# Performance work log

Measured on AMD Instinct MI355X. Metric: run time of the kernel, lower is better.

Reference implementation:

```python
import jax, jax.numpy as jnp
import numpy as np
from jax import lax

# ---- static module constants (the torch module's registered buffers) ----
NRB = 8            # num_radial_basis
RAD = 2.5          # diameter / 2
GRID = 192         # voxel grid extent
N = 200000         # occupied voxels
DIM = 80           # 32x0e + 16x1o
ALPHA = 1.0 / np.sqrt(48.0)   # e3nn path normalization (fan_in = 32 + 16 into each output irrep)

_ax = np.arange(-2.0, 3.0, dtype=np.float32)                        # floor(2.5/1.0)=2 -> 5 taps/axis
LATTICE = np.stack(np.meshgrid(_ax, _ax, _ax, indexing='ij'), -1)   # [5,5,5,3]
PERM = np.arange(125).reshape(5, 5, 5).transpose(2, 1, 0).reshape(-1)  # einsum('xyz...->zyx...') as a flat permutation
OFFS = LATTICE.reshape(-1, 3).astype(np.int32)[PERM]                # voxel offsets, ordered to match permuted kernel


def _radial_emb():
    # soft_one_hot_linspace(..., basis='smooth_finite', cutoff=True)
    d = np.linalg.norm(LATTICE, axis=-1)
    centers = np.linspace(0.0, RAD, NRB + 2)[1:-1]
    step = centers[1] - centers[0]
    t = (d[..., None] - centers) / step
    inside = np.abs(t) < 1.0
    safe = np.where(inside, 1.0 - t * t, 1.0)
    return (1.14136 * np.exp(2.0) * np.where(inside, np.exp(-2.0 / safe), 0.0)).astype(np.float32)

EMB = _radial_emb().reshape(-1, NRB)  # [125, 8]


def _sph():
    # spherical harmonics l=0,1; normalize=True, normalization='component' (|Y_l|^2 = 2l+1)
    n = np.linalg.norm(LATTICE, axis=-1, keepdims=True)
    u = np.where(n > 0, LATTICE / np.maximum(n, 1e-9), 0.0)
    return np.concatenate([np.ones_like(n), np.sqrt(3.0) * u], -1).astype(np.float32)

SH = _sph().reshape(-1, 4)  # [125, 4]


def make_kernel(weight):
    # kernel(): (emb @ weight) / numel(lattice), then tp.right(sh, w) -> [tap, dim_in, dim_out]
    w = jnp.asarray(EMB) @ weight / 125.0        # [125, 2304]
    w1 = w[:, :1024].reshape(125, 32, 32)        # path 0e x 0e -> 0e
    w2 = w[:, 1024:1536].reshape(125, 32, 16)    # path 0e x 1o -> 1o
    w3 = w[:, 1536:1792].reshape(125, 16, 16)    # path 1o x 0e -> 1o
    w4 = w[:, 1792:].reshape(125, 16, 32)        # path 1o x 1o -> 0e (dot product)
    s0 = jnp.asarray(SH[:, 0])
    v = jnp.asarray(SH[:, 1:])
    eye3 = jnp.eye(3, dtype=w.dtype)
    K00 = ALPHA * w1 * s0[:, None, None]                                                  # [125,32,32]
    K01 = ALPHA * jnp.einsum('pik,pm->pikm', w2, v).reshape(125, 32, 48)                  # [125,32,48]
    K11 = ALPHA * jnp.einsum('pik,mn->pimkn', w3 * s0[:, None, None], eye3).reshape(125, 48, 48)
    K10 = (ALPHA / np.sqrt(3.0)) * jnp.einsum('pik,pm->pimk', w4, v).reshape(125, 48, 32)
    K = jnp.concatenate([jnp.concatenate([K00, K01], 2), jnp.concatenate([K10, K11], 2)], 1)
    return K[jnp.asarray(PERM)]  # xyz -> zyx tap order + flatten


def _forward(feats, weight, w_sc0, w_sc1, coords):
    kern = make_kernel(weight)  # [125, 80, 80]
    # residual e3nn Linear: per-irrep channel mixing with 1/sqrt(fan_in) normalization
    sc0 = feats[:, :32] @ (w_sc0 / np.sqrt(32.0))
    sc1 = jnp.einsum('nim,ik->nkm', feats[:, 32:].reshape(-1, 16, 3), w_sc1 / np.sqrt(16.0)).reshape(-1, 48)
    sc = jnp.concatenate([sc0, sc1], -1)
    # Minkowski sparse voxel conv: dense index volume -> per-tap gather / GEMM / accumulate
    n = coords.shape[0]
    idx_vol = jnp.full((GRID, GRID, GRID), -1, jnp.int32)
    idx_vol = idx_vol.at[coords[:, 0], coords[:, 1], coords[:, 2]].set(jnp.arange(n, dtype=jnp.int32))

    def tap(acc, oK):
        off, Ko = oK
        c = coords + off                                  # [N,3] neighbor coords for this tap
        ok = jnp.all((c >= 0) & (c < GRID), axis=1)
        cc = jnp.clip(c, 0, GRID - 1)
        nb = idx_vol[cc[:, 0], cc[:, 1], cc[:, 2]]        # [N] row index or -1
        f = jnp.where((ok & (nb >= 0))[:, None], feats[jnp.maximum(nb, 0)], 0.0)
        return acc + f @ Ko, None

    out, _ = lax.scan(tap, jnp.zeros(feats.shape, feats.dtype), (jnp.asarray(OFFS), kern))
    return sc + out


def setup_inputs() -> dict:
    key = jax.random.key(0)
    k1, k2, k3, k4 = jax.random.split(key, 4)
    rng = np.random.default_rng(0)
    lin = rng.choice(GRID ** 3, size=N, replace=False)  # unique occupied voxels
    coords = np.stack([lin // (GRID * GRID), (lin // GRID) % GRID, lin % GRID], 1).astype(np.int32)
    return {
        'feats': jax.random.normal(k1, (N, DIM), jnp.float32),
        'weight': jax.random.normal(k2, (NRB, 2304), jnp.float32),
        'w_sc0': jax.random.normal(k3, (32, 32), jnp.float32),
        'w_sc1': jax.random.normal(k4, (16, 16), jnp.float32),
        'coords': jnp.asarray(coords),
    }


def reference(feats, weight, w_sc0, w_sc1, coords):
    return _forward(feats, weight, w_sc0, w_sc1, coords)
```

## Files before the change

### kernel.cpp

```cpp
#include <hip/hip_runtime.h>

#define N_PTS 200000
#define GRIDL 192
#define CAP 8192
#define NREG 216
#define RCAP 1152
#define SCAP 96

#define VOL_OFF   0ull
#define VOL_BYTES (192ull*192ull*192ull*4ull)
#define BINS_OFF  28311552ull
#define BCNT_OFF  36503552ull
#define RCNT_OFF  36519552ull
#define PLIST_OFF 36547200ull
#define WBUF_OFF  38537856ull
#define VTAB_OFF  39689856ull
#define A0_OFF    39691856ull
#define A1_OFF    39695952ull

struct TapTable { int p[80]; };
__host__ __device__ constexpr TapTable make_taps() {
    TapTable tt{}; int t = 0;
    for (int a = -2; a <= 2; a++)
        for (int b = -2; b <= 2; b++)
            for (int c = -2; c <= 2; c++) {
                int sq = a*a + b*b + c*c;
                if (sq >= 1 && sq <= 6) tt.p[t++] = (a+2)*25 + (b+2)*5 + (c+2);
            }
    return tt;
}
__device__ const TapTable TAPS = make_taps();

__global__ void prep_kernel(const float* __restrict__ wt, const float* __restrict__ wsc0,
                            const float* __restrict__ wsc1, float* __restrict__ wbuf,
                            float* __restrict__ vtab, float* __restrict__ A0,
                            float* __restrict__ A1) {
    int p = blockIdx.x;
    int dx = p / 25 - 2, dy = (p / 5) % 5 - 2, dz = p % 5 - 2;
    double d = sqrt((double)(dx*dx + dy*dy + dz*dz));
    const double step = 2.5 / 9.0;
    const double cst = 1.14136 * exp(2.0);
    float emb[8];
#pragma unroll
    for (int r = 0; r < 8; r++) {
        double t = (d - (double)(r + 1) * step) / step;
        double tt = t * t;
        emb[r] = (tt < 1.0) ? (float)(cst * exp(-2.0 / (1.0 - tt))) : 0.0f;
    }
    if (threadIdx.x == 0) {
        float inv = (d > 0.0) ? (float)(sqrt(3.0) / d) : 0.0f;
        vtab[p*4+0] = dx * inv; vtab[p*4+1] = dy * inv;
        vtab[p*4+2] = dz * inv; vtab[p*4+3] = 0.0f;
    }
    const float ALPHA = 0.14433756729740643f;
    for (int q = threadIdx.x; q < 2304; q += blockDim.x) {
        float acc = 0.0f;
#pragma unroll
        for (int r = 0; r < 8; r++) acc = fmaf(emb[r], wt[r*2304 + q], acc);
        acc *= (1.0f / 125.0f);
        float val = acc * ((q < 1792) ? ALPHA : (1.0f / 12.0f));
        wbuf[p*2304 + q] = val;
        if (p == 62) {
            if (q < 1024)                   A0[q]        = wsc0[q] * 0.17677669529663687f + val;
            else if (q >= 1536 && q < 1792) A1[q-1536]   = wsc1[q-1536] * 0.25f + val;
        }
    }
}

__global__ __launch_bounds__(256) void scatter_kernel(const int* __restrict__ coords,
        int* __restrict__ vol, int* __restrict__ rcnt_pad, int2* __restrict__ plist) {
    __shared__ int hist[216];
    __shared__ int rbase[216];
    for (int i = threadIdx.x; i < 216; i += 256) hist[i] = 0;
    __syncthreads();
    for (int n = blockIdx.x * 256 + threadIdx.x; n < N_PTS; n += 65536) {
        int x = coords[n*3], y = coords[n*3+1], z = coords[n*3+2];
        vol[(x * GRIDL + y) * GRIDL + z] = n;
        int r = (x >> 5) * 36 + (y >> 5) * 6 + (z >> 5);
        atomicAdd(&hist[r], 1);
    }
    __syncthreads();
    if (threadIdx.x < 216) {
        rbase[threadIdx.x] = atomicAdd(&rcnt_pad[threadIdx.x * 32], hist[threadIdx.x]);
        hist[threadIdx.x] = 0;
    }
    __syncthreads();
    for (int n = blockIdx.x * 256 + threadIdx.x; n < N_PTS; n += 65536) {
        int x = coords[n*3], y = coords[n*3+1], z = coords[n*3+2];
        int r = (x >> 5) * 36 + (y >> 5) * 6 + (z >> 5);
        int j = rbase[r] + atomicAdd(&hist[r], 1);
        if (j < RCAP) plist[r * RCAP + j] = make_int2(n, (x << 16) | (y << 8) | z);
    }
}

__global__ __launch_bounds__(256) void enum_kernel(const int* __restrict__ vol,
        const int* __restrict__ rcnt_pad, const int2* __restrict__ plist,
        int* __restrict__ bcnt_pad, int2* __restrict__ bins) {
    int r = blockIdx.x;
    int cnt = min(rcnt_pad[r * 32], RCAP);
    __shared__ int hist[80];
    __shared__ int tbase[80];
    __shared__ int2 stage[80][SCAP];
    for (int i = threadIdx.x; i < 80; i += 256) hist[i] = 0;
    __syncthreads();
    for (int idx = threadIdx.x; idx < cnt; idx += 256) {
        int2 e = plist[r * RCAP + idx];
        int n = e.x, x = e.y >> 16, y = (e.y >> 8) & 255, z = e.y & 255;
        int t = 0;
#pragma unroll
        for (int a = -2; a <= 2; a++)
#pragma unroll
        for (int b = -2; b <= 2; b++)
#pragma unroll
        for (int c = -2; c <= 2; c++) {
            int sq = a*a + b*b + c*c;
            if (sq < 1 || sq > 6) continue;
            int cx = x + a, cy = y + b, cz = z + c;
            if (((unsigned)cx < 192u) && ((unsigned)cy < 192u) && ((unsigned)cz < 192u)) {
                int nb = vol[(cx * GRIDL + cy) * GRIDL + cz];
                if (nb >= 0) {
                    int j = atomicAdd(&hist[t], 1);
                    if (j < SCAP) stage[t][j] = make_int2(n, nb);
                }
            }
            t++;
        }
    }
    __syncthreads();
    if (threadIdx.x < 80) {
        int c = min(hist[threadIdx.x], SCAP);
        tbase[threadIdx.x] = atomicAdd(&bcnt_pad[TAPS.p[threadIdx.x] * 32], c);
    }
    __syncthreads();
    for (int t = 0; t < 80; t++) {
        int c = min(hist[t], SCAP);
        if (threadIdx.x < c) {
            int slot = tbase[t] + threadIdx.x;
            if (slot < CAP) bins[TAPS.p[t] * CAP + slot] = stage[t][threadIdx.x];
        }
    }
}

__global__ __launch_bounds__(256) void sc_self_kernel(const float* __restrict__ feats,
        const float* __restrict__ A0, const float* __restrict__ A1,
        float* __restrict__ out) {
    __shared__ __align__(16) float sA0[1024];
    __shared__ __align__(16) float sA1[256];
    for (int i = threadIdx.x; i < 1024; i += 256) sA0[i] = A0[i];
    if (threadIdx.x < 256) sA1[threadIdx.x] = A1[threadIdx.x];
    __syncthreads();
    int n = blockIdx.x * 256 + threadIdx.x;
    if (n >= N_PTS) return;
    const float4* fr = (const float4*)(feats + (size_t)n * 80);
    float4* orow = (float4*)(out + (size_t)n * 80);
    float f0[32];
#pragma unroll
    for (int j = 0; j < 8; j++) {
        float4 t = fr[j];
        f0[4*j] = t.x; f0[4*j+1] = t.y; f0[4*j+2] = t.z; f0[4*j+3] = t.w;
    }
    float a0[32];
#pragma unroll
    for (int k = 0; k < 32; k++) a0[k] = 0.0f;
#pragma unroll
    for (int i = 0; i < 32; i++) {
        float fv = f0[i];
#pragma unroll
        for (int k4 = 0; k4 < 8; k4++) {
            float4 w = ((const float4*)sA0)[i*8 + k4];
            a0[4*k4]   = fmaf(fv, w.x, a0[4*k4]);
            a0[4*k4+1] = fmaf(fv, w.y, a0[4*k4+1]);
            a0[4*k4+2] = fmaf(fv, w.z, a0[4*k4+2]);
            a0[4*k4+3] = fmaf(fv, w.w, a0[4*k4+3]);
        }
    }
#pragma unroll
    for (int j = 0; j < 8; j++) orow[j] = make_float4(a0[4*j], a0[4*j+1], a0[4*j+2], a0[4*j+3]);
    float f1[48];
#pragma unroll
    for (int j = 0; j < 12; j++) {
        float4 t = fr[8 + j];
        f1[4*j] = t.x; f1[4*j+1] = t.y; f1[4*j+2] = t.z; f1[4*j+3] = t.w;
    }
    float a1[48];
#pragma unroll
    for (int k = 0; k < 48; k++) a1[k] = 0.0f;
#pragma unroll
    for (int i = 0; i < 16; i++) {
        float fm0 = f1[3*i], fm1 = f1[3*i+1], fm2 = f1[3*i+2];
#pragma unroll
        for (int k4 = 0; k4 < 4; k4++) {
            float4 w = ((const float4*)sA1)[i*4 + k4];
            const float* wp = (const float*)&w;
#pragma unroll
            for (int kk = 0; kk < 4; kk++) {
                int k = 4*k4 + kk;
                a1[3*k]   = fmaf(fm0, wp[kk], a1[3*k]);
                a1[3*k+1] = fmaf(fm1, wp[kk], a1[3*k+1]);
                a1[3*k+2] = fmaf(fm2, wp[kk], a1[3*k+2]);
            }
        }
    }
#pragma unroll
    for (int j = 0; j < 12; j++) orow[8+j] = make_float4(a1[4*j], a1[4*j+1], a1[4*j+2], a1[4*j+3]);
}

__global__ __launch_bounds__(128) void bin_kernel(const float* __restrict__ feats,
        const float* __restrict__ wbuf, const float* __restrict__ vtab,
        const int* __restrict__ bcnt_pad, const int2* __restrict__ bins,
        float* __restrict__ out) {
    int p = blockIdx.x >> 4;
    int chunk = blockIdx.x & 15;
    int cnt = min(bcnt_pad[p * 32], CAP);
    int start = chunk * 512;
    if (start >= cnt) return;

    __shared__ __align__(16) float sW[2304];
    __shared__ float sv[4];
    __shared__ float ystage[2][64][81];
    __shared__ int   nst[2][64];

    for (int i = threadIdx.x; i < 2304; i += 128) sW[i] = wbuf[p*2304 + i];
    if (threadIdx.x < 4) sv[threadIdx.x] = vtab[p*4 + threadIdx.x];
    __syncthreads();

    int wv = threadIdx.x >> 6, lane = threadIdx.x & 63;
    const float4* sW1 = (const float4*)sW;
    const float4* sW2 = (const float4*)(sW + 1024);
    const float4* sW3 = (const float4*)(sW + 1536);
    const float4* sW4 = (const float4*)(sW + 1792);
    float v0 = sv[0], v1 = sv[1], v2 = sv[2];

    for (int it = 0; it < 4; it++) {
        int h = start + it * 128 + threadIdx.x;
        bool act = h < cnt;
        int n = -1, nb = 0;
        if (act) { int2 e = bins[p*CAP + h]; n = e.x; nb = e.y; }

        const float4* fr = (const float4*)(feats + (size_t)nb * 80);
        float f0[32], f1[48];
#pragma unroll
        for (int j = 0; j < 8; j++) {
            float4 t = fr[j];
            f0[4*j] = t.x; f0[4*j+1] = t.y; f0[4*j+2] = t.z; f0[4*j+3] = t.w;
        }
#pragma unroll
        for (int j = 0; j < 12; j++) {
            float4 t = fr[8 + j];
            f1[4*j] = t.x; f1[4*j+1] = t.y; f1[4*j+2] = t.z; f1[4*j+3] = t.w;
        }
        float g[16];
#pragma unroll
        for (int i = 0; i < 16; i++)
            g[i] = f1[3*i]*v0 + f1[3*i+1]*v1 + f1[3*i+2]*v2;

        float a0[32], cc[16];
#pragma unroll
        for (int k = 0; k < 32; k++) a0[k] = 0.0f;
#pragma unroll
        for (int k = 0; k < 16; k++) cc[k] = 0.0f;
#pragma unroll
        for (int i = 0; i < 32; i++) {
            float fv = f0[i];
#pragma unroll
            for (int k4 = 0; k4 < 8; k4++) {
                float4 w = sW1[i*8 + k4];
                a0[4*k4]   = fmaf(fv, w.x, a0[4*k4]);
                a0[4*k4+1] = fmaf(fv, w.y, a0[4*k4+1]);
                a0[4*k4+2] = fmaf(fv, w.z, a0[4*k4+2]);
                a0[4*k4+3] = fmaf(fv, w.w, a0[4*k4+3]);
            }
#pragma unroll
            for (int k4 = 0; k4 < 4; k4++) {
                float4 w = sW2[i*4 + k4];
                cc[4*k4]   = fmaf(fv, w.x, cc[4*k4]);
                cc[4*k4+1] = fmaf(fv, w.y, cc[4*k4+1]);
                cc[4*k4+2] = fmaf(fv, w.z, cc[4*k4+2]);
                cc[4*k4+3] = fmaf(fv, w.w, cc[4*k4+3]);
            }
        }
#pragma unroll
        for (int i = 0; i < 16; i++) {
            float gv = g[i];
#pragma unroll
            for (int k4 = 0; k4 < 8; k4++) {
                float4 w = sW4[i*8 + k4];
                a0[4*k4]   = fmaf(gv, w.x, a0[4*k4]);
                a0[4*k4+1] = fmaf(gv, w.y, a0[4*k4+1]);
                a0[4*k4+2] = fmaf(gv, w.z, a0[4*k4+2]);
                a0[4*k4+3] = fmaf(gv, w.w, a0[4*k4+3]);
            }
        }
#pragma unroll
        for (int k = 0; k < 32; k++) ystage[wv][lane][k] = a0[k];

        float a1[48];
#pragma unroll
        for (int k = 0; k < 16; k++) {
            a1[3*k] = v0 * cc[k]; a1[3*k+1] = v1 * cc[k]; a1[3*k+2] = v2 * cc[k];
        }
#pragma unroll
        for (int i = 0; i < 16; i++) {
            float fm0 = f1[3*i], fm1 = f1[3*i+1], fm2 = f1[3*i+2];
#pragma unroll
            for (int k4 = 0; k4 < 4; k4++) {
                float4 w = sW3[i*4 + k4];
                const float* wp = (const float*)&w;
#pragma unroll
                for (int kk = 0; kk < 4; kk++) {
                    int k = 4*k4 + kk;
                    a1[3*k]   = fmaf(fm0, wp[kk], a1[3*k]);
                    a1[3*k+1] = fmaf(fm1, wp[kk], a1[3*k+1]);
                    a1[3*k+2] = fmaf(fm2, wp[kk], a1[3*k+2]);
                }
            }
        }
#pragma unroll
        for (int k = 0; k < 48; k++) ystage[wv][lane][32 + k] = a1[k];
        nst[wv][lane] = act ? n : -1;
        __syncthreads();

        for (int h2 = 0; h2 < 64; h2++) {
            int nn = nst[wv][h2];
            if (nn < 0) continue;
            float* orow = out + (size_t)nn * 80;
            unsafeAtomicAdd(orow + lane, ystage[wv][h2][lane]);
            if (lane < 16) unsafeAtomicAdd(orow + 64 + lane, ystage[wv][h2][64 + lane]);
        }
        __syncthreads();
    }
}

extern "C" void kernel_launch(void* const* d_in, const int* in_sizes, int n_in,
                              void* d_out, int out_size, void* d_ws, size_t ws_size,
                              hipStream_t stream) {
    const float* feats = (const float*)d_in[0];
    const float* wt    = (const float*)d_in[1];
    const float* wsc0  = (const float*)d_in[2];
    const float* wsc1  = (const float*)d_in[3];
    const int*   coords= (const int*)d_in[4];
    float* out = (float*)d_out;
    char* ws = (char*)d_ws;

    int*   vol      = (int*)(ws + VOL_OFF);
    int2*  bins     = (int2*)(ws + BINS_OFF);
    int*   bcnt_pad = (int*)(ws + BCNT_OFF);
    int*   rcnt_pad = (int*)(ws + RCNT_OFF);
    int2*  plist    = (int2*)(ws + PLIST_OFF);
    float* wbuf     = (float*)(ws + WBUF_OFF);
    float* vtab     = (float*)(ws + VTAB_OFF);
    float* A0       = (float*)(ws + A0_OFF);
    float* A1       = (float*)(ws + A1_OFF);

    hipMemsetAsync(vol, 0xFF, VOL_BYTES, stream);
    hipMemsetAsync(bcnt_pad, 0, 16000 + 27648, stream);

    prep_kernel<<<125, 256, 0, stream>>>(wt, wsc0, wsc1, wbuf, vtab, A0, A1);
    scatter_kernel<<<256, 256, 0, stream>>>(coords, vol, rcnt_pad, plist);
    enum_kernel<<<NREG, 256, 0, stream>>>(vol, rcnt_pad, plist, bcnt_pad, bins);
    sc_self_kernel<<<(N_PTS + 255) / 256, 256, 0, stream>>>(feats, A0, A1, out);
    bin_kernel<<<125 * 16, 128, 0, stream>>>(feats, wbuf, vtab, bcnt_pad, bins, out);
}
```

Before: 472.0 us.

## Replace atomic scatter-add with per-pair staging rows and deterministic gather

The enum kernel now gives every (point, neighbor) pair a unique staging slot through per-block and global prefix counters, and records a per-point header (base, count). The bin kernel writes each per-pair result row to its slot with plain stores instead of float atomics into the output. A new gather kernel fuses the self-connection matmul with a sequential sum of each point's staged rows and writes the output once. This removes atomic contention and read-modify-write traffic, at the cost of a large staging buffer (about 160MB) that is written and then read back. It falls back to the old path when the workspace is too small.

```diff
diff --git a/kernel.cpp b/kernel.cpp
--- a/kernel.cpp
+++ b/kernel.cpp
@@ -6,17 +6,23 @@
 #define NREG 216
 #define RCAP 1152
 #define SCAP 96
+#define HMAX 16
+#define HCAP_TOT 524288
 
 #define VOL_OFF   0ull
 #define VOL_BYTES (192ull*192ull*192ull*4ull)
 #define BINS_OFF  28311552ull
 #define BCNT_OFF  36503552ull
-#define RCNT_OFF  36519552ull
-#define PLIST_OFF 36547200ull
-#define WBUF_OFF  38537856ull
-#define VTAB_OFF  39689856ull
-#define A0_OFF    39691856ull
-#define A1_OFF    39695952ull
+#define GCUR_OFF  36519552ull
+#define RCNT_OFF  36519680ull
+#define PLIST_OFF 36547328ull
+#define WBUF_OFF  38537984ull
+#define VTAB_OFF  39689984ull
+#define A0_OFF    39691984ull
+#define A1_OFF    39696080ull
+#define HDR_OFF   39697104ull
+#define STAGE_OFF 41297104ull
+#define WS_NEED   (STAGE_OFF + (unsigned long long)HCAP_TOT * 320ull)
 
 struct TapTable { int p[80]; };
 __host__ __device__ constexpr TapTable make_taps() {
@@ -93,19 +99,31 @@
     }
 }
 
+template<bool STG>
 __global__ __launch_bounds__(256) void enum_kernel(const int* __restrict__ vol,
         const int* __restrict__ rcnt_pad, const int2* __restrict__ plist,
-        int* __restrict__ bcnt_pad, int2* __restrict__ bins) {
+        int* __restrict__ bcnt_pad, int2* __restrict__ bins,
+        int2* __restrict__ hdr, int* __restrict__ gcur) {
     int r = blockIdx.x;
     int cnt = min(rcnt_pad[r * 32], RCAP);
     __shared__ int hist[80];
     __shared__ int tbase[80];
     __shared__ int2 stage[80][SCAP];
+    __shared__ int2 mh[STG ? 256 * HMAX : 1];
+    __shared__ int blockTot;
+    __shared__ int gbase_s;
     for (int i = threadIdx.x; i < 80; i += 256) hist[i] = 0;
     __syncthreads();
-    for (int idx = threadIdx.x; idx < cnt; idx += 256) {
-        int2 e = plist[r * RCAP + idx];
-        int n = e.x, x = e.y >> 16, y = (e.y >> 8) & 255, z = e.y & 255;
+
+    for (int base = 0; base < cnt; base += 256) {
+        int idx = base + threadIdx.x;
+        bool act = idx < cnt;
+        int n = -1, x = 0, y = 0, z = 0;
+        if (act) {
+            int2 e = plist[r * RCAP + idx];
+            n = e.x; x = e.y >> 16; y = (e.y >> 8) & 255; z = e.y & 255;
+        }
+        int myc = 0;
         int t = 0;
 #pragma unroll
         for (int a = -2; a <= 2; a++)
@@ -116,14 +134,39 @@
             int sq = a*a + b*b + c*c;
             if (sq < 1 || sq > 6) continue;
             int cx = x + a, cy = y + b, cz = z + c;
-            if (((unsigned)cx < 192u) && ((unsigned)cy < 192u) && ((unsigned)cz < 192u)) {
+            if (act && ((unsigned)cx < 192u) && ((unsigned)cy < 192u) && ((unsigned)cz < 192u)) {
                 int nb = vol[(cx * GRIDL + cy) * GRIDL + cz];
                 if (nb >= 0) {
-                    int j = atomicAdd(&hist[t], 1);
-                    if (j < SCAP) stage[t][j] = make_int2(n, nb);
+                    if (STG) {
+                        if (myc < HMAX) mh[threadIdx.x * HMAX + myc] = make_int2(t, nb);
+                        myc++;
+                    } else {
+                        int j = atomicAdd(&hist[t], 1);
+                        if (j < SCAP) stage[t][j] = make_int2(n, nb);
+                    }
                 }
             }
             t++;
+        }
+        if (STG) {
+            myc = min(myc, HMAX);
+            __syncthreads();
+            if (threadIdx.x == 0) blockTot = 0;
+            __syncthreads();
+            int lbase = atomicAdd(&blockTot, myc);
+            __syncthreads();
+            if (threadIdx.x == 0) gbase_s = atomicAdd(gcur, blockTot);
+            __syncthreads();
+            int sbase = gbase_s + lbase;
+            int avail = HCAP_TOT - sbase;
+            int cn = min(myc, max(avail, 0));
+            if (act) hdr[n] = make_int2(sbase, cn);
+            for (int j = 0; j < cn; j++) {
+                int2 e = mh[threadIdx.x * HMAX + j];
+                int k = atomicAdd(&hist[e.x], 1);
+                if (k < SCAP) stage[e.x][k] = make_int2(sbase + j, e.y);
+            }
+            __syncthreads();
         }
     }
     __syncthreads();
@@ -132,11 +175,11 @@
         tbase[threadIdx.x] = atomicAdd(&bcnt_pad[TAPS.p[threadIdx.x] * 32], c);
     }
     __syncthreads();
-    for (int t = 0; t < 80; t++) {
-        int c = min(hist[t], SCAP);
+    for (int t2 = 0; t2 < 80; t2++) {
+        int c = min(hist[t2], SCAP);
         if (threadIdx.x < c) {
-            int slot = tbase[t] + threadIdx.x;
-            if (slot < CAP) bins[TAPS.p[t] * CAP + slot] = stage[t][threadIdx.x];
+            int slot = tbase[t2] + threadIdx.x;
+            if (slot < CAP) bins[TAPS.p[t2] * CAP + slot] = stage[t2][threadIdx.x];
         }
     }
 }
@@ -205,10 +248,11 @@
     for (int j = 0; j < 12; j++) orow[8+j] = make_float4(a1[4*j], a1[4*j+1], a1[4*j+2], a1[4*j+3]);
 }
 
+template<bool STG>
 __global__ __launch_bounds__(128) void bin_kernel(const float* __restrict__ feats,
         const float* __restrict__ wbuf, const float* __restrict__ vtab,
         const int* __restrict__ bcnt_pad, const int2* __restrict__ bins,
-        float* __restrict__ out) {
+        float* __restrict__ stg, float* __restrict__ out) {
     int p = blockIdx.x >> 4;
     int chunk = blockIdx.x & 15;
     int cnt = min(bcnt_pad[p * 32], CAP);
@@ -218,7 +262,7 @@
     __shared__ __align__(16) float sW[2304];
     __shared__ float sv[4];
     __shared__ float ystage[2][64][81];
-    __shared__ int   nst[2][64];
+    __shared__ int   dst[2][64];
 
     for (int i = threadIdx.x; i < 2304; i += 128) sW[i] = wbuf[p*2304 + i];
     if (threadIdx.x < 4) sv[threadIdx.x] = vtab[p*4 + threadIdx.x];
@@ -234,8 +278,8 @@
     for (int it = 0; it < 4; it++) {
         int h = start + it * 128 + threadIdx.x;
         bool act = h < cnt;
-        int n = -1, nb = 0;
-        if (act) { int2 e = bins[p*CAP + h]; n = e.x; nb = e.y; }
+        int d = -1, nb = 0;
+        if (act) { int2 e = bins[p*CAP + h]; d = e.x; nb = e.y; }
 
         const float4* fr = (const float4*)(feats + (size_t)nb * 80);
         float f0[32], f1[48];
@@ -317,18 +361,104 @@
         }
 #pragma unroll
         for (int k = 0; k < 48; k++) ystage[wv][lane][32 + k] = a1[k];
-        nst[wv][lane] = act ? n : -1;
+        dst[wv][lane] = act ? d : -1;
         __syncthreads();
 
         for (int h2 = 0; h2 < 64; h2++) {
-            int nn = nst[wv][h2];
-            if (nn < 0) continue;
-            float* orow = out + (size_t)nn * 80;
-            unsafeAtomicAdd(orow + lane, ystage[wv][h2][lane]);
-            if (lane < 16) unsafeAtomicAdd(orow + 64 + lane, ystage[wv][h2][64 + lane]);
+            int dd = dst[wv][h2];
+            if (dd < 0) continue;
+            if (STG) {
+                float* row = stg + (size_t)dd * 80;
+                row[lane] = ystage[wv][h2][lane];
+                if (lane < 16) row[64 + lane] = ystage[wv][h2][64 + lane];
+            } else {
+                float* orow = out + (size_t)dd * 80;
+                unsafeAtomicAdd(orow + lane, ystage[wv][h2][lane]);
+                if (lane < 16) unsafeAtomicAdd(orow + 64 + lane, ystage[wv][h2][64 + lane]);
+            }
         }
         __syncthreads();
     }
+}
+
+__global__ __launch_bounds__(256) void gather_kernel(const float* __restrict__ feats,
+        const float* __restrict__ A0, const float* __restrict__ A1,
+        const int2* __restrict__ hdr, const float* __restrict__ stg,
+        float* __restrict__ out) {
+    __shared__ __align__(16) float sA0[1024];
+    __shared__ __align__(16) float sA1[256];
+    for (int i = threadIdx.x; i < 1024; i += 256) sA0[i] = A0[i];
+    if (threadIdx.x < 256) sA1[threadIdx.x] = A1[threadIdx.x];
+    __syncthreads();
+    int n = blockIdx.x * 256 + threadIdx.x;
+    if (n >= N_PTS) return;
+    int2 h = hdr[n];
+    const float4* fr = (const float4*)(feats + (size_t)n * 80);
+    float a0[32], a1[48];
+    {
+        float f0[32];
+#pragma unroll
+        for (int j = 0; j < 8; j++) {
+            float4 t = fr[j];
+            f0[4*j] = t.x; f0[4*j+1] = t.y; f0[4*j+2] = t.z; f0[4*j+3] = t.w;
+        }
+#pragma unroll
+        for (int k = 0; k < 32; k++) a0[k] = 0.0f;
+#pragma unroll
+        for (int i = 0; i < 32; i++) {
+            float fv = f0[i];
+#pragma unroll
+            for (int k4 = 0; k4 < 8; k4++) {
+                float4 w = ((const float4*)sA0)[i*8 + k4];
+                a0[4*k4]   = fmaf(fv, w.x, a0[4*k4]);
+                a0[4*k4+1] = fmaf(fv, w.y, a0[4*k4+1]);
+                a0[4*k4+2] = fmaf(fv, w.z, a0[4*k4+2]);
+                a0[4*k4+3] = fmaf(fv, w.w, a0[4*k4+3]);
+            }
+        }
+        float f1[48];
+#pragma unroll
+        for (int j = 0; j < 12; j++) {
+            float4 t = fr[8 + j];
+            f1[4*j] = t.x; f1[4*j+1] = t.y; f1[4*j+2] = t.z; f1[4*j+3] = t.w;
+        }
+#pragma unroll
+        for (int k = 0; k < 48; k++) a1[k] = 0.0f;
+#pragma unroll
+        for (int i = 0; i < 16; i++) {
+            float fm0 = f1[3*i], fm1 = f1[3*i+1], fm2 = f1[3*i+2];
+#pragma unroll
+            for (int k4 = 0; k4 < 4; k4++) {
+                float4 w = ((const float4*)sA1)[i*4 + k4];
+                const float* wp = (const float*)&w;
+#pragma unroll
+                for (int kk = 0; kk < 4; kk++) {
+                    int k = 4*k4 + kk;
+                    a1[3*k]   = fmaf(fm0, wp[kk], a1[3*k]);
+                    a1[3*k+1] = fmaf(fm1, wp[kk], a1[3*k+1]);
+                    a1[3*k+2] = fmaf(fm2, wp[kk], a1[3*k+2]);
+                }
+            }
+        }
+    }
+    for (int j = 0; j < h.y; j++) {
+        const float4* rp = (const float4*)(stg + (size_t)(h.x + j) * 80);
+#pragma unroll
+        for (int q = 0; q < 8; q++) {
+            float4 t = rp[q];
+            a0[4*q] += t.x; a0[4*q+1] += t.y; a0[4*q+2] += t.z; a0[4*q+3] += t.w;
+        }
+#pragma unroll
+        for (int q = 0; q < 12; q++) {
+            float4 t = rp[8 + q];
+            a1[4*q] += t.x; a1[4*q+1] += t.y; a1[4*q+2] += t.z; a1[4*q+3] += t.w;
+        }
+    }
+    float4* orow = (float4*)(out + (size_t)n * 80);
+#pragma unroll
+    for (int j = 0; j < 8; j++)  orow[j]   = make_float4(a0[4*j], a0[4*j+1], a0[4*j+2], a0[4*j+3]);
+#pragma unroll
+    for (int j = 0; j < 12; j++) orow[8+j] = make_float4(a1[4*j], a1[4*j+1], a1[4*j+2], a1[4*j+3]);
 }
 
 extern "C" void kernel_launch(void* const* d_in, const int* in_sizes, int n_in,
@@ -345,19 +475,30 @@
     int*   vol      = (int*)(ws + VOL_OFF);
     int2*  bins     = (int2*)(ws + BINS_OFF);
     int*   bcnt_pad = (int*)(ws + BCNT_OFF);
+    int*   gcur     = (int*)(ws + GCUR_OFF);
     int*   rcnt_pad = (int*)(ws + RCNT_OFF);
     int2*  plist    = (int2*)(ws + PLIST_OFF);
     float* wbuf     = (float*)(ws + WBUF_OFF);
     float* vtab     = (float*)(ws + VTAB_OFF);
     float* A0       = (float*)(ws + A0_OFF);
     float* A1       = (float*)(ws + A1_OFF);
+    int2*  hdr      = (int2*)(ws + HDR_OFF);
+    float* stg      = (float*)(ws + STAGE_OFF);
+
+    bool staging = (unsigned long long)ws_size >= WS_NEED;
 
     hipMemsetAsync(vol, 0xFF, VOL_BYTES, stream);
-    hipMemsetAsync(bcnt_pad, 0, 16000 + 27648, stream);
+    hipMemsetAsync(bcnt_pad, 0, 16000 + 128 + 27648, stream);
 
     prep_kernel<<<125, 256, 0, stream>>>(wt, wsc0, wsc1, wbuf, vtab, A0, A1);
     scatter_kernel<<<256, 256, 0, stream>>>(coords, vol, rcnt_pad, plist);
-    enum_kernel<<<NREG, 256, 0, stream>>>(vol, rcnt_pad, plist, bcnt_pad, bins);
-    sc_self_kernel<<<(N_PTS + 255) / 256, 256, 0, stream>>>(feats, A0, A1, out);
-    bin_kernel<<<125 * 16, 128, 0, stream>>>(feats, wbuf, vtab, bcnt_pad, bins, out);
-}
+    if (staging) {
+        enum_kernel<true><<<NREG, 256, 0, stream>>>(vol, rcnt_pad, plist, bcnt_pad, bins, hdr, gcur);
+        bin_kernel<true><<<125 * 16, 128, 0, stream>>>(feats, wbuf, vtab, bcnt_pad, bins, stg, out);
+        gather_kernel<<<(N_PTS + 255) / 256, 256, 0, stream>>>(feats, A0, A1, hdr, stg, out);
+    } else {
+        enum_kernel<false><<<NREG, 256, 0, stream>>>(vol, rcnt_pad, plist, bcnt_pad, bins, hdr, gcur);
+        sc_self_kernel<<<(N_PTS + 255) / 256, 256, 0, stream>>>(feats, A0, A1, out);
+        bin_kernel<false><<<125 * 16, 128, 0, stream>>>(feats, wbuf, vtab, bcnt_pad, bins, stg, out);
+    }
+}
```

Result: slower. 514.9 us (+9.1%).

## Split neighbor enumeration across more blocks and halve bin_kernel staging LDS

Applied to the files above, without the earlier changes.

The enumeration kernel now launches nine 128-thread blocks per spatial region instead of one 256-thread block, each block handling one 128-point slice, so more blocks can run the neighbor lookups concurrently. Per-tap staging shrinks to 32 entries per block, and the writeout spreads taps across warps. bin_kernel stages outputs in two phases of 32 rows to halve the shared staging buffer, which may raise occupancy but adds barriers. Zero-count atomics are skipped. SCAP of 32 per slice could truncate pairs if a tap gets more than 32 hits in a slice, though that is unlikely at this point density.

```diff
diff --git a/kernel.cpp b/kernel.cpp
--- a/kernel.cpp
+++ b/kernel.cpp
@@ -5,7 +5,8 @@
 #define CAP 8192
 #define NREG 216
 #define RCAP 1152
-#define SCAP 96
+#define NSLICE 9
+#define SCAP 32
 
 #define VOL_OFF   0ull
 #define VOL_BYTES (192ull*192ull*192ull*4ull)
@@ -81,7 +82,8 @@
     }
     __syncthreads();
     if (threadIdx.x < 216) {
-        rbase[threadIdx.x] = atomicAdd(&rcnt_pad[threadIdx.x * 32], hist[threadIdx.x]);
+        int c = hist[threadIdx.x];
+        rbase[threadIdx.x] = c ? atomicAdd(&rcnt_pad[threadIdx.x * 32], c) : 0;
         hist[threadIdx.x] = 0;
     }
     __syncthreads();
@@ -93,50 +95,58 @@
     }
 }
 
-__global__ __launch_bounds__(256) void enum_kernel(const int* __restrict__ vol,
+__global__ __launch_bounds__(128) void enum_kernel(const int* __restrict__ vol,
         const int* __restrict__ rcnt_pad, const int2* __restrict__ plist,
         int* __restrict__ bcnt_pad, int2* __restrict__ bins) {
-    int r = blockIdx.x;
+    int r = blockIdx.x / NSLICE, s = blockIdx.x % NSLICE;
     int cnt = min(rcnt_pad[r * 32], RCAP);
+    int lo = s * 128, hi = min(cnt, lo + 128);
+    if (lo >= hi) return;
+    __shared__ int2 stage[80][SCAP];
     __shared__ int hist[80];
     __shared__ int tbase[80];
-    __shared__ int2 stage[80][SCAP];
-    for (int i = threadIdx.x; i < 80; i += 256) hist[i] = 0;
-    __syncthreads();
-    for (int idx = threadIdx.x; idx < cnt; idx += 256) {
+    if (threadIdx.x < 80) hist[threadIdx.x] = 0;
+    __syncthreads();
+
+    int idx = lo + threadIdx.x;
+    bool act = idx < hi;
+    int n = -1, x = 0, y = 0, z = 0;
+    if (act) {
         int2 e = plist[r * RCAP + idx];
-        int n = e.x, x = e.y >> 16, y = (e.y >> 8) & 255, z = e.y & 255;
-        int t = 0;
-#pragma unroll
-        for (int a = -2; a <= 2; a++)
-#pragma unroll
-        for (int b = -2; b <= 2; b++)
-#pragma unroll
-        for (int c = -2; c <= 2; c++) {
-            int sq = a*a + b*b + c*c;
-            if (sq < 1 || sq > 6) continue;
-            int cx = x + a, cy = y + b, cz = z + c;
-            if (((unsigned)cx < 192u) && ((unsigned)cy < 192u) && ((unsigned)cz < 192u)) {
-                int nb = vol[(cx * GRIDL + cy) * GRIDL + cz];
-                if (nb >= 0) {
-                    int j = atomicAdd(&hist[t], 1);
-                    if (j < SCAP) stage[t][j] = make_int2(n, nb);
-                }
-            }
-            t++;
-        }
+        n = e.x; x = e.y >> 16; y = (e.y >> 8) & 255; z = e.y & 255;
+    }
+    int t = 0;
+#pragma unroll
+    for (int a = -2; a <= 2; a++)
+#pragma unroll
+    for (int b = -2; b <= 2; b++)
+#pragma unroll
+    for (int c = -2; c <= 2; c++) {
+        int sq = a*a + b*b + c*c;
+        if (sq < 1 || sq > 6) continue;
+        int cx = x + a, cy = y + b, cz = z + c;
+        if (act && ((unsigned)cx < 192u) && ((unsigned)cy < 192u) && ((unsigned)cz < 192u)) {
+            int nb = vol[(cx * GRIDL + cy) * GRIDL + cz];
+            if (nb >= 0) {
+                int j = atomicAdd(&hist[t], 1);
+                if (j < SCAP) stage[t][j] = make_int2(n, nb);
+            }
+        }
+        t++;
     }
     __syncthreads();
     if (threadIdx.x < 80) {
         int c = min(hist[threadIdx.x], SCAP);
-        tbase[threadIdx.x] = atomicAdd(&bcnt_pad[TAPS.p[threadIdx.x] * 32], c);
-    }
-    __syncthreads();
-    for (int t = 0; t < 80; t++) {
-        int c = min(hist[t], SCAP);
-        if (threadIdx.x < c) {
-            int slot = tbase[t] + threadIdx.x;
-            if (slot < CAP) bins[TAPS.p[t] * CAP + slot] = stage[t][threadIdx.x];
+        tbase[threadIdx.x] = c ? atomicAdd(&bcnt_pad[TAPS.p[threadIdx.x] * 32], c) : 0;
+    }
+    __syncthreads();
+    int g = threadIdx.x >> 5, l = threadIdx.x & 31;
+    for (int q = 0; q < 20; q++) {
+        int t2 = g * 20 + q;
+        int c = min(hist[t2], SCAP);
+        if (l < c) {
+            int pos = tbase[t2] + l;
+            if (pos < CAP) bins[TAPS.p[t2] * CAP + pos] = stage[t2][l];
         }
     }
 }
@@ -217,8 +227,8 @@
 
     __shared__ __align__(16) float sW[2304];
     __shared__ float sv[4];
-    __shared__ float ystage[2][64][81];
-    __shared__ int   nst[2][64];
+    __shared__ float ys[2][32][81];
+    __shared__ int   dst[2][64];
 
     for (int i = threadIdx.x; i < 2304; i += 128) sW[i] = wbuf[p*2304 + i];
     if (threadIdx.x < 4) sv[threadIdx.x] = vtab[p*4 + threadIdx.x];
@@ -291,9 +301,6 @@
                 a0[4*k4+3] = fmaf(gv, w.w, a0[4*k4+3]);
             }
         }
-#pragma unroll
-        for (int k = 0; k < 32; k++) ystage[wv][lane][k] = a0[k];
-
         float a1[48];
 #pragma unroll
         for (int k = 0; k < 16; k++) {
@@ -315,19 +322,27 @@
                 }
             }
         }
-#pragma unroll
-        for (int k = 0; k < 48; k++) ystage[wv][lane][32 + k] = a1[k];
-        nst[wv][lane] = act ? n : -1;
-        __syncthreads();
-
-        for (int h2 = 0; h2 < 64; h2++) {
-            int nn = nst[wv][h2];
-            if (nn < 0) continue;
-            float* orow = out + (size_t)nn * 80;
-            unsafeAtomicAdd(orow + lane, ystage[wv][h2][lane]);
-            if (lane < 16) unsafeAtomicAdd(orow + 64 + lane, ystage[wv][h2][64 + lane]);
-        }
-        __syncthreads();
+        dst[wv][lane] = act ? n : -1;
+
+#pragma unroll
+        for (int ph = 0; ph < 2; ph++) {
+            if ((lane >> 5) == ph) {
+                int rr = lane & 31;
+#pragma unroll
+                for (int k = 0; k < 32; k++) ys[wv][rr][k] = a0[k];
+#pragma unroll
+                for (int k = 0; k < 48; k++) ys[wv][rr][32 + k] = a1[k];
+            }
+            __syncthreads();
+            for (int h2 = 0; h2 < 32; h2++) {
+                int nn = dst[wv][ph * 32 + h2];
+                if (nn < 0) continue;
+                float* orow = out + (size_t)nn * 80;
+                unsafeAtomicAdd(orow + lane, ys[wv][h2][lane]);
+                if (lane < 16) unsafeAtomicAdd(orow + 64 + lane, ys[wv][h2][64 + lane]);
+            }
+            __syncthreads();
+        }
     }
 }
 
@@ -357,7 +372,7 @@
 
     prep_kernel<<<125, 256, 0, stream>>>(wt, wsc0, wsc1, wbuf, vtab, A0, A1);
     scatter_kernel<<<256, 256, 0, stream>>>(coords, vol, rcnt_pad, plist);
-    enum_kernel<<<NREG, 256, 0, stream>>>(vol, rcnt_pad, plist, bcnt_pad, bins);
+    enum_kernel<<<NREG * NSLICE, 128, 0, stream>>>(vol, rcnt_pad, plist, bcnt_pad, bins);
     sc_self_kernel<<<(N_PTS + 255) / 256, 256, 0, stream>>>(feats, A0, A1, out);
     bin_kernel<<<125 * 16, 128, 0, stream>>>(feats, wbuf, vtab, bcnt_pad, bins, out);
 }
```

Result: slower. 500.8 us (+6.1%).
